# Performance work log

Measured on AMD Instinct MI355X. Metric: run time of the kernel, lower is better.

## Reference

```python
import jax, jax.numpy as jnp
import numpy as np

B, S, C, V, D, H, F, L, SEL = 16, 512, 16, 20000, 512, 8, 2048, 2, 64


def _pos_table(d, max_len):
    # sinusoidal table with a zero row prepended (index 0 = padding)
    pos = np.arange(max_len)[:, None].astype(np.float64)
    j = np.arange(d)[None, :]
    ang = pos / np.power(10000.0, 2 * (j // 2) / d)
    pe = np.zeros((max_len, d))
    pe[:, 0::2] = np.sin(ang[:, 0::2])
    pe[:, 1::2] = np.cos(ang[:, 1::2])
    return jnp.asarray(np.concatenate([np.zeros((1, d)), pe], axis=0), dtype=jnp.float32)


def _ln(x, g, b, eps):
    mu = jnp.mean(x, -1, keepdims=True)
    var = jnp.mean(jnp.square(x - mu), -1, keepdims=True)
    return (x - mu) * jax.lax.rsqrt(var + eps) * g + b


def _forward(event_code, input_len, mask, mask_code, seq_time_step, event_failure_sys, event_failure_user,
             emb, bias_emb, sel_W, sel_b, time_W, time_b,
             Wq, bq, Wk, bk, Wv, bv, Wo, bo, ln1_g, ln1_b, W1, b1, W2, b2, ln2_g, ln2_b):
    Bb, Ss, Cc = event_code.shape
    Dd = emb.shape[1]
    # time feature: 1 - tanh((Dense64(t/7200))^2) -> Dense(D)
    t = seq_time_step[..., None] / 7200.0
    time_feature = (1.0 - jnp.tanh(jnp.square(t @ sel_W + sel_b))) @ time_W + time_b  # [B,S,D]
    # masked sum of per-code embeddings (public-dataset path: failure bits unused)
    act_emb = emb[event_code]                                   # [B,S,C,D]
    out = jnp.sum(act_emb * mask_code, axis=2) + bias_emb       # [B,S,D]
    out = out + time_feature
    # positional encoding gated by real lengths
    pe = _pos_table(Dd, Ss)
    pos = jnp.arange(1, Ss + 1)
    ind_pos = jnp.where(pos[None, :] <= input_len[:, None], pos[None, :], 0)  # [B,S]
    out = out + pe[ind_pos]
    dh = Dd // H
    scale = dh ** -0.5
    for l in range(Wq.shape[0]):
        residual = out
        # NOTE: original uses a raw reshape [B,S,H*dh] -> [B*H,-1,dh]; reproduced exactly.
        q = (out @ Wq[l] + bq[l]).reshape(Bb * H, -1, dh)
        k = (out @ Wk[l] + bk[l]).reshape(Bb * H, -1, dh)
        v = (out @ Wv[l] + bv[l]).reshape(Bb * H, -1, dh)
        # NOTE: original computes tf.where(attn_mask,-inf,attn) but discards the result,
        # so no padding mask is actually applied; reproduced faithfully.
        attn = jax.nn.softmax(jnp.einsum('bqd,bkd->bqk', q, k) * scale, axis=2)
        ctx = jnp.matmul(attn, v).reshape(Bb, -1, H * dh)
        out = _ln(residual + ctx @ Wo[l] + bo[l], ln1_g[l], ln1_b[l], 1e-3)
        ffn = jax.nn.relu(out @ W1[l] + b1[l]) @ W2[l] + b2[l]
        out = _ln(out + ffn, ln2_g[l], ln2_b[l], 1e-6)
    return out


def setup_inputs():
    ks = jax.random.split(jax.random.key(0), 40)
    g = lambda i, shp: jax.random.normal(ks[i], shp, dtype=jnp.float32) * 0.02
    return {
        "event_code": jax.random.randint(ks[0], (B, S, C), 0, V),
        "mask": jnp.ones((B, S), jnp.float32),
        "mask_code": jnp.ones((B, S, C, 1), jnp.float32),
        "seq_time_step": jax.random.uniform(ks[1], (B, S), dtype=jnp.float32) * 7200.0,
        "event_failure_sys": jax.random.uniform(ks[2], (B, S), dtype=jnp.float32),
        "event_failure_user": jax.random.uniform(ks[3], (B, S), dtype=jnp.float32),
        "input_len": jax.random.randint(ks[4], (B,), 1, S + 1),
        "emb": g(5, (V, D)),
        "bias_emb": g(6, (D,)),
        "sel_W": g(7, (1, SEL)), "sel_b": jnp.zeros((SEL,), jnp.float32),
        "time_W": g(8, (SEL, D)), "time_b": jnp.zeros((D,), jnp.float32),
        "Wq": g(9, (L, D, D)), "bq": jnp.zeros((L, D), jnp.float32),
        "Wk": g(10, (L, D, D)), "bk": jnp.zeros((L, D), jnp.float32),
        "Wv": g(11, (L, D, D)), "bv": jnp.zeros((L, D), jnp.float32),
        "Wo": g(12, (L, D, D)), "bo": jnp.zeros((L, D), jnp.float32),
        "ln1_g": jnp.ones((L, D), jnp.float32), "ln1_b": jnp.zeros((L, D), jnp.float32),
        "W1": g(13, (L, D, F)), "b1": jnp.zeros((L, F), jnp.float32),
        "W2": g(14, (L, F, D)), "b2": jnp.zeros((L, D), jnp.float32),
        "ln2_g": jnp.ones((L, D), jnp.float32), "ln2_b": jnp.zeros((L, D), jnp.float32),
    }


def reference(event_code, mask, mask_code, seq_time_step, event_failure_sys, event_failure_user, input_len,
              emb, bias_emb, sel_W, sel_b, time_W, time_b,
              Wq, bq, Wk, bk, Wv, bv, Wo, bo, ln1_g, ln1_b, W1, b1, W2, b2, ln2_g, ln2_b):
    return _forward(event_code, input_len, mask, mask_code, seq_time_step, event_failure_sys, event_failure_user,
                    emb, bias_emb, sel_W, sel_b, time_W, time_b,
                    Wq, bq, Wk, bk, Wv, bv, Wo, bo, ln1_g, ln1_b, W1, b1, W2, b2, ln2_g, ln2_b)
```

## Files before the change

### kernel.cpp

```cpp
#include <hip/hip_runtime.h>
#include <math.h>

#define BB   16
#define SS   512
#define CC   16
#define DD   512
#define DH   64
#define FF   2048
#define LL   2
#define NTOK (BB*SS)
#define NG   (BB*8)
#define GRP  (SS*DH)
#define ST   72

typedef unsigned short u16;
typedef __attribute__((ext_vector_type(8))) short bf16x8;
typedef __attribute__((ext_vector_type(4))) float f32x4;

__device__ __forceinline__ u16 f2bf(float x) {
    unsigned u = __float_as_uint(x);
    u = (u + 0x7fffu + ((u >> 16) & 1u)) >> 16;
    return (u16)u;
}
__device__ __forceinline__ float bf2f(u16 h) {
    return __uint_as_float(((unsigned)h) << 16);
}
__device__ __forceinline__ void gload16(const void* g, void* l) {
    __builtin_amdgcn_global_load_lds((const __attribute__((address_space(1))) void*)g,
                                     (__attribute__((address_space(3))) void*)l, 16, 0, 0);
}

__global__ __launch_bounds__(256) void cvt_weight(
    const float* __restrict__ W, u16* __restrict__ Th, u16* __restrict__ Tl,
    int K, int N)
{
    const long moff = (long)blockIdx.z * K * N;
    W  += moff; Th += moff; Tl += moff;
    const int n0 = blockIdx.x * 32, k0 = blockIdx.y * 32;
    __shared__ float T[32][33];
    const int t = threadIdx.x;

    {
        const int lk = t >> 3, ln4 = (t & 7) * 4;
        float4 w4 = *(const float4*)&W[(long)(k0 + lk) * N + n0 + ln4];
        T[ln4 + 0][lk] = w4.x; T[ln4 + 1][lk] = w4.y;
        T[ln4 + 2][lk] = w4.z; T[ln4 + 3][lk] = w4.w;
    }
    __syncthreads();
    {
        const int nn = t >> 3, kq = (t & 7) * 4;
        float v0 = T[nn][kq + 0], v1 = T[nn][kq + 1];
        float v2 = T[nn][kq + 2], v3 = T[nn][kq + 3];
        ushort4 hh, ll;
        hh.x = f2bf(v0); ll.x = f2bf(v0 - bf2f(hh.x));
        hh.y = f2bf(v1); ll.y = f2bf(v1 - bf2f(hh.y));
        hh.z = f2bf(v2); ll.z = f2bf(v2 - bf2f(hh.z));
        hh.w = f2bf(v3); ll.w = f2bf(v3 - bf2f(hh.w));
        long o = (long)(n0 + nn) * K + k0 + kq;
        *(ushort4*)&Th[o] = hh;
        *(ushort4*)&Tl[o] = ll;
    }
}

__global__ __launch_bounds__(512) void embed_kernel(
    const int*   __restrict__ event_code,
    const float* __restrict__ mask_code,
    const float* __restrict__ seq_time,
    const int*   __restrict__ input_len,
    const float* __restrict__ emb,
    const float* __restrict__ bias_emb,
    const float* __restrict__ sel_W,
    const float* __restrict__ sel_b,
    const float* __restrict__ time_W,
    const float* __restrict__ time_b,
    float* __restrict__ out, u16* __restrict__ oh)
{
    const int tok = blockIdx.x;
    const int b   = tok >> 9;
    const int s   = tok & 511;
    const int d   = threadIdx.x;

    __shared__ float f[64];
    __shared__ int   codes[16];
    __shared__ float mcode[16];

    if (d < 64) {
        float t = seq_time[tok] * (1.0f / 7200.0f);
        float h = t * sel_W[d] + sel_b[d];
        f[d] = 1.0f - tanhf(h * h);
    }
    if (d >= 64 && d < 80) {
        int c = d - 64;
        codes[c] = event_code[tok * CC + c];
        mcode[c] = mask_code[tok * CC + c];
    }
    __syncthreads();

    float acc = bias_emb[d] + time_b[d];
    #pragma unroll
    for (int c = 0; c < CC; ++c)
        acc += emb[(long)codes[c] * DD + d] * mcode[c];
    #pragma unroll 8
    for (int j = 0; j < 64; ++j)
        acc += f[j] * time_W[j * DD + d];

    int pos = s + 1;
    if (pos <= input_len[b]) {
        int p = pos - 1;
        float e    = (float)(d & ~1) * (1.0f / 512.0f);
        float invf = exp2f(-13.287712379549449f * e);
        float ang  = (float)p * invf;
        acc += (d & 1) ? cosf(ang) : sinf(ang);
    }
    long o = (long)tok * DD + d;
    out[o] = acc;
    oh[o] = f2bf(acc);
}

template<int BN, bool RELU, bool RES, int EMIT>
__global__ __launch_bounds__(256) void mgemm(
    const u16* __restrict__ A,
    const u16* __restrict__ Bh, const u16* __restrict__ Bl,
    const float* __restrict__ bias, const float* __restrict__ res,
    float* __restrict__ C, u16* __restrict__ Cb,
    int N, int K)
{
    constexpr int WN = BN / 2;
    constexpr int NI = WN / 16;
    __shared__ __align__(16) u16 A_s[128 * 32];
    __shared__ __align__(16) u16 Bh_s[BN * 32];
    __shared__ __align__(16) u16 Bl_s[BN * 32];

    const int tid  = threadIdx.x;
    const int wid  = tid >> 6, lane = tid & 63;
    const int wr   = wid >> 1, wc = wid & 1;
    const int l4   = lane >> 4, l15 = lane & 15;

    const int bid  = blockIdx.x + gridDim.x * blockIdx.y;
    const int xcd  = bid & 7;
    const int slot = bid >> 3;
    const int ppx  = gridDim.y >> 3;
    const int by   = xcd * ppx + slot / gridDim.x;
    const int bx   = slot % gridDim.x;
    const int m0   = by * 128, n0 = bx * BN;
    const int sr   = lane >> 2, sc = lane & 3;

    f32x4 acc[4][NI];
    #pragma unroll
    for (int mi = 0; mi < 4; ++mi)
        #pragma unroll
        for (int ni = 0; ni < NI; ++ni)
            acc[mi][ni] = (f32x4){0.f, 0.f, 0.f, 0.f};

    for (int k0 = 0; k0 < K; k0 += 32) {
        #pragma unroll
        for (int i = 0; i < 2; ++i) {
            int rr = wid * 32 + i * 16;
            long go = (long)(m0 + rr + sr) * K + k0 + sc * 8;
            gload16(A + go, &A_s[rr * 32]);
        }
        #pragma unroll
        for (int i = 0; i < BN / 64; ++i) {
            int rr = wid * (BN / 4) + i * 16;
            long go = (long)(n0 + rr + sr) * K + k0 + sc * 8;
            gload16(Bh + go, &Bh_s[rr * 32]);
            gload16(Bl + go, &Bl_s[rr * 32]);
        }
        __syncthreads();

        bf16x8 af[4], bh[NI], bl[NI];
        #pragma unroll
        for (int mi = 0; mi < 4; ++mi) {
            int row = wr * 64 + mi * 16 + l15;
            af[mi] = *(const bf16x8*)&A_s[row * 32 + l4 * 8];
        }
        #pragma unroll
        for (int ni = 0; ni < NI; ++ni) {
            int row = wc * WN + ni * 16 + l15;
            bh[ni] = *(const bf16x8*)&Bh_s[row * 32 + l4 * 8];
            bl[ni] = *(const bf16x8*)&Bl_s[row * 32 + l4 * 8];
        }
        #pragma unroll
        for (int mi = 0; mi < 4; ++mi)
            #pragma unroll
            for (int ni = 0; ni < NI; ++ni) {
                acc[mi][ni] = __builtin_amdgcn_mfma_f32_16x16x32_bf16(af[mi], bh[ni], acc[mi][ni], 0, 0, 0);
                acc[mi][ni] = __builtin_amdgcn_mfma_f32_16x16x32_bf16(af[mi], bl[ni], acc[mi][ni], 0, 0, 0);
            }
        __syncthreads();
    }

    #pragma unroll
    for (int mi = 0; mi < 4; ++mi)
        #pragma unroll
        for (int ni = 0; ni < NI; ++ni) {
            int col = n0 + wc * WN + ni * 16 + l15;
            float bv = bias[col];
            #pragma unroll
            for (int r = 0; r < 4; ++r) {
                int row = m0 + wr * 64 + mi * 16 + l4 * 4 + r;
                long off = (long)row * N + col;
                float v = acc[mi][ni][r] + bv;
                if (RES) v += res[off];
                if (RELU) v = fmaxf(v, 0.f);
                if (EMIT == 2) Cb[off] = f2bf(v);
                else           C[off]  = v;
            }
        }
}

__global__ __launch_bounds__(256) void attn_kernel(
    const u16* __restrict__ Qg, const u16* __restrict__ Kg, const u16* __restrict__ Vg,
    u16* __restrict__ Oh)
{
    const int bid = blockIdx.x;
    const int xcd = bid & 7, slot = bid >> 3;
    const int g   = xcd * 16 + (slot >> 3);
    const int qt  = slot & 7;
    const int tid = threadIdx.x;
    const int w   = tid >> 6;
    const int lane = tid & 63;
    const int l4  = lane >> 4, l15 = lane & 15;

    __shared__ __align__(16) u16 Qs[64 * ST];
    __shared__ __align__(16) u16 Ks[64 * ST];
    __shared__ __align__(16) u16 Vt[64 * ST];
    __shared__ __align__(16) u16 Ps[64 * ST];

    const long gbase = (long)g * GRP;

    {
        const u16* src = Qg + gbase + (long)qt * 64 * 64;
        #pragma unroll
        for (int i = 0; i < 2; ++i) {
            int slot2 = tid + i * 256;
            int row = slot2 >> 3, c8 = slot2 & 7;
            *(int4*)&Qs[row * ST + c8 * 8] = *(const int4*)&src[row * 64 + c8 * 8];
        }
    }
    __syncthreads();

    const bf16x8 qf0 = *(const bf16x8*)&Qs[(w * 16 + l15) * ST + l4 * 8];
    const bf16x8 qf1 = *(const bf16x8*)&Qs[(w * 16 + l15) * ST + 32 + l4 * 8];

    f32x4 oacc[4];
    #pragma unroll
    for (int db = 0; db < 4; ++db) oacc[db] = (f32x4){0.f, 0.f, 0.f, 0.f};
    float mrun = -3e38f, lrun = 0.f;

    const int k0t = (tid >> 4) * 4;
    const int d0t = (tid & 15) * 4;

    for (int kt = 0; kt < 8; ++kt) {
        const u16* ksrc = Kg + gbase + (long)kt * 4096;
        const u16* vsrc = Vg + gbase + (long)kt * 4096;
        #pragma unroll
        for (int i = 0; i < 2; ++i) {
            int slot2 = tid + i * 256;
            int row = slot2 >> 3, c8 = slot2 & 7;
            *(int4*)&Ks[row * ST + c8 * 8] = *(const int4*)&ksrc[row * 64 + c8 * 8];
        }
        {
            ushort4 r0 = *(const ushort4*)&vsrc[(k0t + 0) * 64 + d0t];
            ushort4 r1 = *(const ushort4*)&vsrc[(k0t + 1) * 64 + d0t];
            ushort4 r2 = *(const ushort4*)&vsrc[(k0t + 2) * 64 + d0t];
            ushort4 r3 = *(const ushort4*)&vsrc[(k0t + 3) * 64 + d0t];
            ushort4 t0, t1, t2, t3;
            t0.x = r0.x; t0.y = r1.x; t0.z = r2.x; t0.w = r3.x;
            t1.x = r0.y; t1.y = r1.y; t1.z = r2.y; t1.w = r3.y;
            t2.x = r0.z; t2.y = r1.z; t2.z = r2.z; t2.w = r3.z;
            t3.x = r0.w; t3.y = r1.w; t3.z = r2.w; t3.w = r3.w;
            *(ushort4*)&Vt[(d0t + 0) * ST + k0t] = t0;
            *(ushort4*)&Vt[(d0t + 1) * ST + k0t] = t1;
            *(ushort4*)&Vt[(d0t + 2) * ST + k0t] = t2;
            *(ushort4*)&Vt[(d0t + 3) * ST + k0t] = t3;
        }
        __syncthreads();

        f32x4 sacc[4];
        #pragma unroll
        for (int kb = 0; kb < 4; ++kb) {
            bf16x8 a0 = *(const bf16x8*)&Ks[(kb * 16 + l15) * ST + l4 * 8];
            bf16x8 a1 = *(const bf16x8*)&Ks[(kb * 16 + l15) * ST + 32 + l4 * 8];
            f32x4 z = (f32x4){0.f, 0.f, 0.f, 0.f};
            z = __builtin_amdgcn_mfma_f32_16x16x32_bf16(a0, qf0, z, 0, 0, 0);
            z = __builtin_amdgcn_mfma_f32_16x16x32_bf16(a1, qf1, z, 0, 0, 0);
            sacc[kb] = z;
        }

        float pm = -3e38f;
        #pragma unroll
        for (int kb = 0; kb < 4; ++kb)
            #pragma unroll
            for (int r = 0; r < 4; ++r)
                pm = fmaxf(pm, sacc[kb][r]);
        pm *= 0.125f;
        pm = fmaxf(pm, __shfl_xor(pm, 16));
        pm = fmaxf(pm, __shfl_xor(pm, 32));
        float mn   = fmaxf(mrun, pm);
        float corr = __expf(mrun - mn);
        float psum = 0.f;
        u16 pb[16];
        #pragma unroll
        for (int kb = 0; kb < 4; ++kb)
            #pragma unroll
            for (int r = 0; r < 4; ++r) {
                float p = __expf(sacc[kb][r] * 0.125f - mn);
                u16 b = f2bf(p);
                pb[kb * 4 + r] = b;
                psum += bf2f(b);
            }
        psum += __shfl_xor(psum, 16);
        psum += __shfl_xor(psum, 32);
        lrun = lrun * corr + psum;
        mrun = mn;

        #pragma unroll
        for (int kb = 0; kb < 4; ++kb)
            #pragma unroll
            for (int r = 0; r < 4; ++r)
                Ps[(w * 16 + l15) * ST + kb * 16 + l4 * 4 + r] = pb[kb * 4 + r];

        float cr[4];
        #pragma unroll
        for (int r = 0; r < 4; ++r) cr[r] = __shfl(corr, l4 * 4 + r);
        #pragma unroll
        for (int db = 0; db < 4; ++db)
            #pragma unroll
            for (int r = 0; r < 4; ++r)
                oacc[db][r] *= cr[r];

        asm volatile("s_waitcnt lgkmcnt(0)" ::: "memory");
        __builtin_amdgcn_sched_barrier(0);
        bf16x8 pa0 = *(const bf16x8*)&Ps[(w * 16 + l15) * ST + l4 * 8];
        bf16x8 pa1 = *(const bf16x8*)&Ps[(w * 16 + l15) * ST + 32 + l4 * 8];
        #pragma unroll
        for (int db = 0; db < 4; ++db) {
            bf16x8 v0 = *(const bf16x8*)&Vt[(db * 16 + l15) * ST + l4 * 8];
            bf16x8 v1 = *(const bf16x8*)&Vt[(db * 16 + l15) * ST + 32 + l4 * 8];
            oacc[db] = __builtin_amdgcn_mfma_f32_16x16x32_bf16(pa0, v0, oacc[db], 0, 0, 0);
            oacc[db] = __builtin_amdgcn_mfma_f32_16x16x32_bf16(pa1, v1, oacc[db], 0, 0, 0);
        }
        __syncthreads();
    }

    float li[4];
    #pragma unroll
    for (int r = 0; r < 4; ++r) li[r] = 1.0f / __shfl(lrun, l4 * 4 + r);
    #pragma unroll
    for (int db = 0; db < 4; ++db)
        #pragma unroll
        for (int r = 0; r < 4; ++r) {
            float val = oacc[db][r] * li[r];
            long addr = gbase + (long)(qt * 64 + w * 16 + l4 * 4 + r) * 64 + db * 16 + l15;
            Oh[addr] = f2bf(val);
        }
}

__global__ __launch_bounds__(256) void ln_kernel(
    const float* __restrict__ X,
    const float* __restrict__ gam,
    const float* __restrict__ bet,
    float* __restrict__ Y, u16* __restrict__ Yh,
    float eps)
{
    const int row = blockIdx.x;
    const int tid = threadIdx.x;
    const float* x = X + (long)row * DD;

    float x0 = x[tid], x1 = x[tid + 256];
    __shared__ float ws4[4];
    const int wid = tid >> 6, lane = tid & 63;

    float sum = x0 + x1;
    #pragma unroll
    for (int off = 32; off > 0; off >>= 1) sum += __shfl_down(sum, off, 64);
    if (lane == 0) ws4[wid] = sum;
    __syncthreads();
    float mean = (ws4[0] + ws4[1] + ws4[2] + ws4[3]) * (1.0f / 512.0f);
    __syncthreads();

    float d0 = x0 - mean, d1 = x1 - mean;
    float s2 = d0 * d0 + d1 * d1;
    #pragma unroll
    for (int off = 32; off > 0; off >>= 1) s2 += __shfl_down(s2, off, 64);
    if (lane == 0) ws4[wid] = s2;
    __syncthreads();
    float var = (ws4[0] + ws4[1] + ws4[2] + ws4[3]) * (1.0f / 512.0f);
    float inv = rsqrtf(var + eps);

    float o0 = d0 * inv * gam[tid]       + bet[tid];
    float o1 = d1 * inv * gam[tid + 256] + bet[tid + 256];
    long b0 = (long)row * DD + tid;
    Y[b0] = o0;  Y[b0 + 256] = o1;
    Yh[b0] = f2bf(o0);
    Yh[b0 + 256] = f2bf(o1);
}

extern "C" void kernel_launch(void* const* d_in, const int* in_sizes, int n_in,
                              void* d_out, int out_size, void* d_ws, size_t ws_size,
                              hipStream_t stream)
{
    const int*   event_code = (const int*)  d_in[0];
    const float* mask_code  = (const float*)d_in[2];
    const float* seq_time   = (const float*)d_in[3];
    const int*   input_len  = (const int*)  d_in[6];
    const float* emb        = (const float*)d_in[7];
    const float* bias_emb   = (const float*)d_in[8];
    const float* sel_W      = (const float*)d_in[9];
    const float* sel_b      = (const float*)d_in[10];
    const float* time_W     = (const float*)d_in[11];
    const float* time_b     = (const float*)d_in[12];
    const float* Wq  = (const float*)d_in[13];
    const float* bq  = (const float*)d_in[14];
    const float* Wk  = (const float*)d_in[15];
    const float* bk  = (const float*)d_in[16];
    const float* Wv  = (const float*)d_in[17];
    const float* bv  = (const float*)d_in[18];
    const float* Wo  = (const float*)d_in[19];
    const float* bo  = (const float*)d_in[20];
    const float* ln1g = (const float*)d_in[21];
    const float* ln1b = (const float*)d_in[22];
    const float* W1  = (const float*)d_in[23];
    const float* b1  = (const float*)d_in[24];
    const float* W2  = (const float*)d_in[25];
    const float* b2  = (const float*)d_in[26];
    const float* ln2g = (const float*)d_in[27];
    const float* ln2b = (const float*)d_in[28];

    float* ws = (float*)d_ws;
    const long ND = (long)NTOK * DD;
    const long NF = (long)NTOK * FF;
    float* x = ws;
    float* y = ws + ND;
    u16* q16 = (u16*)(ws + 2 * ND);
    u16* k16 = q16 + ND;
    u16* v16 = k16 + ND;
    u16* a16 = v16 + ND;
    u16* h16 = a16 + ND;
    u16* wq_h = h16 + NF;
    const long SZQ = (long)LL * DD * DD, SZF = (long)LL * DD * FF;
    u16* wq_l = wq_h + SZQ;
    u16* wk_h = wq_l + SZQ;  u16* wk_l = wk_h + SZQ;
    u16* wv_h = wk_l + SZQ;  u16* wv_l = wv_h + SZQ;
    u16* wo_h = wv_l + SZQ;  u16* wo_l = wo_h + SZQ;
    u16* w1_h = wo_l + SZQ;  u16* w1_l = w1_h + SZF;
    u16* w2_h = w1_l + SZF;  u16* w2_l = w2_h + SZF;

    cvt_weight<<<dim3(DD/32, DD/32, LL), 256, 0, stream>>>(Wq, wq_h, wq_l, DD, DD);
    cvt_weight<<<dim3(DD/32, DD/32, LL), 256, 0, stream>>>(Wk, wk_h, wk_l, DD, DD);
    cvt_weight<<<dim3(DD/32, DD/32, LL), 256, 0, stream>>>(Wv, wv_h, wv_l, DD, DD);
    cvt_weight<<<dim3(DD/32, DD/32, LL), 256, 0, stream>>>(Wo, wo_h, wo_l, DD, DD);
    cvt_weight<<<dim3(FF/32, DD/32, LL), 256, 0, stream>>>(W1, w1_h, w1_l, DD, FF);
    cvt_weight<<<dim3(DD/32, FF/32, LL), 256, 0, stream>>>(W2, w2_h, w2_l, FF, DD);

    embed_kernel<<<NTOK, 512, 0, stream>>>(event_code, mask_code, seq_time, input_len,
                                           emb, bias_emb, sel_W, sel_b, time_W, time_b,
                                           x, a16);

    const dim3 gN512(DD / 64, NTOK / 128);
    const dim3 gN2048(FF / 128, NTOK / 128);

    for (int l = 0; l < LL; ++l) {
        const u16* qh = wq_h + (long)l * DD * DD;  const u16* ql = wq_l + (long)l * DD * DD;
        const u16* kh = wk_h + (long)l * DD * DD;  const u16* kl = wk_l + (long)l * DD * DD;
        const u16* vh = wv_h + (long)l * DD * DD;  const u16* vl = wv_l + (long)l * DD * DD;
        const u16* oh = wo_h + (long)l * DD * DD;  const u16* ol = wo_l + (long)l * DD * DD;
        const u16* f1h = w1_h + (long)l * DD * FF; const u16* f1l = w1_l + (long)l * DD * FF;
        const u16* f2h = w2_h + (long)l * FF * DD; const u16* f2l = w2_l + (long)l * FF * DD;

        mgemm<64,false,false,2><<<gN512, 256, 0, stream>>>(a16, qh, ql, bq + l*DD, nullptr, nullptr, q16, DD, DD);
        mgemm<64,false,false,2><<<gN512, 256, 0, stream>>>(a16, kh, kl, bk + l*DD, nullptr, nullptr, k16, DD, DD);
        mgemm<64,false,false,2><<<gN512, 256, 0, stream>>>(a16, vh, vl, bv + l*DD, nullptr, nullptr, v16, DD, DD);

        attn_kernel<<<NG * 8, 256, 0, stream>>>(q16, k16, v16, a16);

        mgemm<64,false,true,0><<<gN512, 256, 0, stream>>>(a16, oh, ol, bo + l*DD, x, y, nullptr, DD, DD);
        ln_kernel<<<NTOK, 256, 0, stream>>>(y, ln1g + l*DD, ln1b + l*DD, y, a16, 1e-3f);

        mgemm<128,true,false,2><<<gN2048, 256, 0, stream>>>(a16, f1h, f1l, b1 + l*FF, nullptr, nullptr, h16, FF, DD);
        mgemm<64,false,true,0><<<gN512, 256, 0, stream>>>(h16, f2h, f2l, b2 + l*DD, y, x, nullptr, DD, FF);

        float* lnout = (l == LL - 1) ? (float*)d_out : x;
        ln_kernel<<<NTOK, 256, 0, stream>>>(x, ln2g + l*DD, ln2b + l*DD, lnout, a16, 1e-6f);
    }
}
```

Measured before the change: 617.0 us.

## Fuse QKV GEMMs, double-buffer GEMM LDS loads, use bf16 embedding table

The separate Q, K and V projection GEMMs become one N=1536 GEMM over a packed weight, with a segmented epilogue that routes columns to the three outputs. The GEMM main loop gains double-buffered LDS staging with explicit vmcnt waits, so the next tile's global loads overlap the MFMA work. The Q/K/V/O weight conversions merge into one launch. The embedding table is converted to bf16 and the embed kernel processes two features per thread with vector loads. Converting the 20000x512 table every call adds a full pass over it, and bf16 embeddings lose precision compared with the fp32 gather.

```diff
diff --git a/kernel.cpp b/kernel.cpp
--- a/kernel.cpp
+++ b/kernel.cpp
@@ -8,6 +8,7 @@
 #define DH   64
 #define FF   2048
 #define LL   2
+#define VV   20000
 #define NTOK (BB*SS)
 #define NG   (BB*8)
 #define GRP  (SS*DH)
@@ -30,16 +31,58 @@
                                      (__attribute__((address_space(3))) void*)l, 16, 0, 0);
 }
 
+__global__ __launch_bounds__(256) void cvt_qkvo(
+    const float* __restrict__ Wq, const float* __restrict__ Wk,
+    const float* __restrict__ Wv, const float* __restrict__ Wo,
+    u16* __restrict__ qkv_h, u16* __restrict__ qkv_l,
+    u16* __restrict__ o_h,   u16* __restrict__ o_l)
+{
+    const int z = blockIdx.z;
+    const int which = z >> 1, l = z & 1;
+    const float* W = (which == 0) ? Wq : (which == 1) ? Wk : (which == 2) ? Wv : Wo;
+    W += (long)l * DD * DD;
+    u16 *Th, *Tl;
+    if (which < 3) {
+        long off = (long)l * 1536 * DD + (long)which * DD * DD;
+        Th = qkv_h + off; Tl = qkv_l + off;
+    } else {
+        long off = (long)l * DD * DD;
+        Th = o_h + off;   Tl = o_l + off;
+    }
+    const int n0 = blockIdx.x * 32, k0 = blockIdx.y * 32;
+    __shared__ float T[32][33];
+    const int t = threadIdx.x;
+    {
+        const int lk = t >> 3, ln4 = (t & 7) * 4;
+        float4 w4 = *(const float4*)&W[(long)(k0 + lk) * DD + n0 + ln4];
+        T[ln4 + 0][lk] = w4.x; T[ln4 + 1][lk] = w4.y;
+        T[ln4 + 2][lk] = w4.z; T[ln4 + 3][lk] = w4.w;
+    }
+    __syncthreads();
+    {
+        const int nn = t >> 3, kq = (t & 7) * 4;
+        float v0 = T[nn][kq + 0], v1 = T[nn][kq + 1];
+        float v2 = T[nn][kq + 2], v3 = T[nn][kq + 3];
+        ushort4 hh, ll;
+        hh.x = f2bf(v0); ll.x = f2bf(v0 - bf2f(hh.x));
+        hh.y = f2bf(v1); ll.y = f2bf(v1 - bf2f(hh.y));
+        hh.z = f2bf(v2); ll.z = f2bf(v2 - bf2f(hh.z));
+        hh.w = f2bf(v3); ll.w = f2bf(v3 - bf2f(hh.w));
+        long o = (long)(n0 + nn) * DD + k0 + kq;
+        *(ushort4*)&Th[o] = hh;
+        *(ushort4*)&Tl[o] = ll;
+    }
+}
+
 __global__ __launch_bounds__(256) void cvt_weight(
     const float* __restrict__ W, u16* __restrict__ Th, u16* __restrict__ Tl,
     int K, int N)
 {
     const long moff = (long)blockIdx.z * K * N;
-    W  += moff; Th += moff; Tl += moff;
+    W += moff; Th += moff; Tl += moff;
     const int n0 = blockIdx.x * 32, k0 = blockIdx.y * 32;
     __shared__ float T[32][33];
     const int t = threadIdx.x;
-
     {
         const int lk = t >> 3, ln4 = (t & 7) * 4;
         float4 w4 = *(const float4*)&W[(long)(k0 + lk) * N + n0 + ln4];
@@ -62,12 +105,22 @@
     }
 }
 
-__global__ __launch_bounds__(512) void embed_kernel(
+__global__ __launch_bounds__(256) void cvt_emb(const float* __restrict__ E,
+                                               u16* __restrict__ E16)
+{
+    long i = ((long)blockIdx.x * 256 + threadIdx.x) * 4;
+    float4 v = *(const float4*)&E[i];
+    ushort4 o;
+    o.x = f2bf(v.x); o.y = f2bf(v.y); o.z = f2bf(v.z); o.w = f2bf(v.w);
+    *(ushort4*)&E16[i] = o;
+}
+
+__global__ __launch_bounds__(256) void embed_kernel(
     const int*   __restrict__ event_code,
     const float* __restrict__ mask_code,
     const float* __restrict__ seq_time,
     const int*   __restrict__ input_len,
-    const float* __restrict__ emb,
+    const u16*   __restrict__ emb16,
     const float* __restrict__ bias_emb,
     const float* __restrict__ sel_W,
     const float* __restrict__ sel_b,
@@ -78,58 +131,73 @@
     const int tok = blockIdx.x;
     const int b   = tok >> 9;
     const int s   = tok & 511;
-    const int d   = threadIdx.x;
+    const int t2  = threadIdx.x;
+    const int d   = t2 * 2;
 
     __shared__ float f[64];
     __shared__ int   codes[16];
     __shared__ float mcode[16];
 
-    if (d < 64) {
+    if (t2 < 64) {
         float t = seq_time[tok] * (1.0f / 7200.0f);
-        float h = t * sel_W[d] + sel_b[d];
-        f[d] = 1.0f - tanhf(h * h);
-    }
-    if (d >= 64 && d < 80) {
-        int c = d - 64;
+        float h = t * sel_W[t2] + sel_b[t2];
+        f[t2] = 1.0f - tanhf(h * h);
+    }
+    if (t2 >= 64 && t2 < 80) {
+        int c = t2 - 64;
         codes[c] = event_code[tok * CC + c];
         mcode[c] = mask_code[tok * CC + c];
     }
     __syncthreads();
 
-    float acc = bias_emb[d] + time_b[d];
-    #pragma unroll
-    for (int c = 0; c < CC; ++c)
-        acc += emb[(long)codes[c] * DD + d] * mcode[c];
+    float acc0 = bias_emb[d]     + time_b[d];
+    float acc1 = bias_emb[d + 1] + time_b[d + 1];
+    #pragma unroll
+    for (int c = 0; c < CC; ++c) {
+        unsigned pk = *(const unsigned*)&emb16[(long)codes[c] * DD + d];
+        acc0 += bf2f((u16)(pk & 0xffffu)) * mcode[c];
+        acc1 += bf2f((u16)(pk >> 16))     * mcode[c];
+    }
     #pragma unroll 8
-    for (int j = 0; j < 64; ++j)
-        acc += f[j] * time_W[j * DD + d];
+    for (int j = 0; j < 64; ++j) {
+        float2 tw = *(const float2*)&time_W[j * DD + d];
+        acc0 += f[j] * tw.x;
+        acc1 += f[j] * tw.y;
+    }
 
     int pos = s + 1;
     if (pos <= input_len[b]) {
         int p = pos - 1;
-        float e    = (float)(d & ~1) * (1.0f / 512.0f);
+        float e    = (float)d * (1.0f / 512.0f);
         float invf = exp2f(-13.287712379549449f * e);
         float ang  = (float)p * invf;
-        acc += (d & 1) ? cosf(ang) : sinf(ang);
+        acc0 += sinf(ang);
+        acc1 += cosf(ang);
     }
     long o = (long)tok * DD + d;
-    out[o] = acc;
-    oh[o] = f2bf(acc);
-}
-
-template<int BN, bool RELU, bool RES, int EMIT>
+    float2 o2; o2.x = acc0; o2.y = acc1;
+    *(float2*)&out[o] = o2;
+    unsigned pk = (unsigned)f2bf(acc0) | ((unsigned)f2bf(acc1) << 16);
+    *(unsigned*)&oh[o] = pk;
+}
+
+template<int BN, bool RELU, bool RES, int EMIT, bool SEG3>
 __global__ __launch_bounds__(256) void mgemm(
     const u16* __restrict__ A,
     const u16* __restrict__ Bh, const u16* __restrict__ Bl,
-    const float* __restrict__ bias, const float* __restrict__ res,
-    float* __restrict__ C, u16* __restrict__ Cb,
+    const float* __restrict__ bias0, const float* __restrict__ bias1,
+    const float* __restrict__ bias2,
+    const float* __restrict__ res,
+    float* __restrict__ C,
+    u16* __restrict__ O0, u16* __restrict__ O1, u16* __restrict__ O2,
     int N, int K)
 {
-    constexpr int WN = BN / 2;
-    constexpr int NI = WN / 16;
-    __shared__ __align__(16) u16 A_s[128 * 32];
-    __shared__ __align__(16) u16 Bh_s[BN * 32];
-    __shared__ __align__(16) u16 Bl_s[BN * 32];
+    constexpr int WN  = BN / 2;
+    constexpr int NI  = WN / 16;
+    constexpr int LPW = 2 + 2 * (BN / 64);
+    __shared__ __align__(16) u16 A_s[2][128 * 32];
+    __shared__ __align__(16) u16 Bh_s[2][BN * 32];
+    __shared__ __align__(16) u16 Bl_s[2][BN * 32];
 
     const int tid  = threadIdx.x;
     const int wid  = tid >> 6, lane = tid & 63;
@@ -145,41 +213,57 @@
     const int m0   = by * 128, n0 = bx * BN;
     const int sr   = lane >> 2, sc = lane & 3;
 
-    f32x4 acc[4][NI];
-    #pragma unroll
-    for (int mi = 0; mi < 4; ++mi)
-        #pragma unroll
-        for (int ni = 0; ni < NI; ++ni)
-            acc[mi][ni] = (f32x4){0.f, 0.f, 0.f, 0.f};
-
-    for (int k0 = 0; k0 < K; k0 += 32) {
+    auto STAGE = [&](int bufi, int k0) {
         #pragma unroll
         for (int i = 0; i < 2; ++i) {
             int rr = wid * 32 + i * 16;
             long go = (long)(m0 + rr + sr) * K + k0 + sc * 8;
-            gload16(A + go, &A_s[rr * 32]);
+            gload16(A + go, &A_s[bufi][rr * 32]);
         }
         #pragma unroll
         for (int i = 0; i < BN / 64; ++i) {
             int rr = wid * (BN / 4) + i * 16;
             long go = (long)(n0 + rr + sr) * K + k0 + sc * 8;
-            gload16(Bh + go, &Bh_s[rr * 32]);
-            gload16(Bl + go, &Bl_s[rr * 32]);
-        }
-        __syncthreads();
+            gload16(Bh + go, &Bh_s[bufi][rr * 32]);
+            gload16(Bl + go, &Bl_s[bufi][rr * 32]);
+        }
+    };
+
+    f32x4 acc[4][NI];
+    #pragma unroll
+    for (int mi = 0; mi < 4; ++mi)
+        #pragma unroll
+        for (int ni = 0; ni < NI; ++ni)
+            acc[mi][ni] = (f32x4){0.f, 0.f, 0.f, 0.f};
+
+    STAGE(0, 0);
+    const int nt = K / 32;
+    for (int t = 0; t < nt; ++t) {
+        const int cur = t & 1;
+        if (t + 1 < nt) {
+            STAGE(cur ^ 1, (t + 1) * 32);
+            asm volatile("s_waitcnt vmcnt(%0)" :: "i"(LPW) : "memory");
+        } else {
+            asm volatile("s_waitcnt vmcnt(0)" ::: "memory");
+        }
+        __builtin_amdgcn_s_barrier();
 
         bf16x8 af[4], bh[NI], bl[NI];
         #pragma unroll
         for (int mi = 0; mi < 4; ++mi) {
             int row = wr * 64 + mi * 16 + l15;
-            af[mi] = *(const bf16x8*)&A_s[row * 32 + l4 * 8];
+            af[mi] = *(const bf16x8*)&A_s[cur][row * 32 + l4 * 8];
         }
         #pragma unroll
         for (int ni = 0; ni < NI; ++ni) {
             int row = wc * WN + ni * 16 + l15;
-            bh[ni] = *(const bf16x8*)&Bh_s[row * 32 + l4 * 8];
-            bl[ni] = *(const bf16x8*)&Bl_s[row * 32 + l4 * 8];
-        }
+            bh[ni] = *(const bf16x8*)&Bh_s[cur][row * 32 + l4 * 8];
+            bl[ni] = *(const bf16x8*)&Bl_s[cur][row * 32 + l4 * 8];
+        }
+        asm volatile("s_waitcnt lgkmcnt(0)" ::: "memory");
+        __builtin_amdgcn_sched_barrier(0);
+        __builtin_amdgcn_s_barrier();
+
         #pragma unroll
         for (int mi = 0; mi < 4; ++mi)
             #pragma unroll
@@ -187,23 +271,27 @@
                 acc[mi][ni] = __builtin_amdgcn_mfma_f32_16x16x32_bf16(af[mi], bh[ni], acc[mi][ni], 0, 0, 0);
                 acc[mi][ni] = __builtin_amdgcn_mfma_f32_16x16x32_bf16(af[mi], bl[ni], acc[mi][ni], 0, 0, 0);
             }
-        __syncthreads();
     }
 
     #pragma unroll
     for (int mi = 0; mi < 4; ++mi)
         #pragma unroll
         for (int ni = 0; ni < NI; ++ni) {
-            int col = n0 + wc * WN + ni * 16 + l15;
-            float bv = bias[col];
+            int colg = n0 + wc * WN + ni * 16 + l15;
+            int seg  = SEG3 ? (colg >> 9) : 0;
+            int coll = SEG3 ? (colg & 511) : colg;
+            const float* bp = SEG3 ? (seg == 0 ? bias0 : seg == 1 ? bias1 : bias2) : bias0;
+            u16* op = SEG3 ? (seg == 0 ? O0 : seg == 1 ? O1 : O2) : O0;
+            const int ost = SEG3 ? 512 : N;
+            float bv = bp[coll];
             #pragma unroll
             for (int r = 0; r < 4; ++r) {
                 int row = m0 + wr * 64 + mi * 16 + l4 * 4 + r;
-                long off = (long)row * N + col;
+                long off = (long)row * ost + coll;
                 float v = acc[mi][ni][r] + bv;
                 if (RES) v += res[off];
                 if (RELU) v = fmaxf(v, 0.f);
-                if (EMIT == 2) Cb[off] = f2bf(v);
+                if (EMIT == 2) op[off] = f2bf(v);
                 else           C[off]  = v;
             }
         }
@@ -438,48 +526,52 @@
     u16* v16 = k16 + ND;
     u16* a16 = v16 + ND;
     u16* h16 = a16 + ND;
-    u16* wq_h = h16 + NF;
+    u16* e16 = h16 + NF;
+    u16* wqkv_h = e16 + (long)VV * DD;
+    const long SZ3 = (long)LL * 1536 * DD;
     const long SZQ = (long)LL * DD * DD, SZF = (long)LL * DD * FF;
-    u16* wq_l = wq_h + SZQ;
-    u16* wk_h = wq_l + SZQ;  u16* wk_l = wk_h + SZQ;
-    u16* wv_h = wk_l + SZQ;  u16* wv_l = wv_h + SZQ;
-    u16* wo_h = wv_l + SZQ;  u16* wo_l = wo_h + SZQ;
-    u16* w1_h = wo_l + SZQ;  u16* w1_l = w1_h + SZF;
-    u16* w2_h = w1_l + SZF;  u16* w2_l = w2_h + SZF;
-
-    cvt_weight<<<dim3(DD/32, DD/32, LL), 256, 0, stream>>>(Wq, wq_h, wq_l, DD, DD);
-    cvt_weight<<<dim3(DD/32, DD/32, LL), 256, 0, stream>>>(Wk, wk_h, wk_l, DD, DD);
-    cvt_weight<<<dim3(DD/32, DD/32, LL), 256, 0, stream>>>(Wv, wv_h, wv_l, DD, DD);
-    cvt_weight<<<dim3(DD/32, DD/32, LL), 256, 0, stream>>>(Wo, wo_h, wo_l, DD, DD);
+    u16* wqkv_l = wqkv_h + SZ3;
+    u16* wo_h = wqkv_l + SZ3;  u16* wo_l = wo_h + SZQ;
+    u16* w1_h = wo_l + SZQ;    u16* w1_l = w1_h + SZF;
+    u16* w2_h = w1_l + SZF;    u16* w2_l = w2_h + SZF;
+
+    cvt_qkvo<<<dim3(16, 16, 8), 256, 0, stream>>>(Wq, Wk, Wv, Wo, wqkv_h, wqkv_l, wo_h, wo_l);
     cvt_weight<<<dim3(FF/32, DD/32, LL), 256, 0, stream>>>(W1, w1_h, w1_l, DD, FF);
     cvt_weight<<<dim3(DD/32, FF/32, LL), 256, 0, stream>>>(W2, w2_h, w2_l, FF, DD);
-
-    embed_kernel<<<NTOK, 512, 0, stream>>>(event_code, mask_code, seq_time, input_len,
-                                           emb, bias_emb, sel_W, sel_b, time_W, time_b,
+    cvt_emb<<<(VV * DD) / 1024, 256, 0, stream>>>(emb, e16);
+
+    embed_kernel<<<NTOK, 256, 0, stream>>>(event_code, mask_code, seq_time, input_len,
+                                           e16, bias_emb, sel_W, sel_b, time_W, time_b,
                                            x, a16);
 
+    const dim3 gQKV(1536 / 64, NTOK / 128);
     const dim3 gN512(DD / 64, NTOK / 128);
     const dim3 gN2048(FF / 128, NTOK / 128);
 
     for (int l = 0; l < LL; ++l) {
-        const u16* qh = wq_h + (long)l * DD * DD;  const u16* ql = wq_l + (long)l * DD * DD;
-        const u16* kh = wk_h + (long)l * DD * DD;  const u16* kl = wk_l + (long)l * DD * DD;
-        const u16* vh = wv_h + (long)l * DD * DD;  const u16* vl = wv_l + (long)l * DD * DD;
+        const u16* qkvh = wqkv_h + (long)l * 1536 * DD;
+        const u16* qkvl = wqkv_l + (long)l * 1536 * DD;
         const u16* oh = wo_h + (long)l * DD * DD;  const u16* ol = wo_l + (long)l * DD * DD;
         const u16* f1h = w1_h + (long)l * DD * FF; const u16* f1l = w1_l + (long)l * DD * FF;
         const u16* f2h = w2_h + (long)l * FF * DD; const u16* f2l = w2_l + (long)l * FF * DD;
 
-        mgemm<64,false,false,2><<<gN512, 256, 0, stream>>>(a16, qh, ql, bq + l*DD, nullptr, nullptr, q16, DD, DD);
-        mgemm<64,false,false,2><<<gN512, 256, 0, stream>>>(a16, kh, kl, bk + l*DD, nullptr, nullptr, k16, DD, DD);
-        mgemm<64,false,false,2><<<gN512, 256, 0, stream>>>(a16, vh, vl, bv + l*DD, nullptr, nullptr, v16, DD, DD);
+        mgemm<64,false,false,2,true><<<gQKV, 256, 0, stream>>>(
+            a16, qkvh, qkvl, bq + l*DD, bk + l*DD, bv + l*DD, nullptr,
+            nullptr, q16, k16, v16, 1536, DD);
 
         attn_kernel<<<NG * 8, 256, 0, stream>>>(q16, k16, v16, a16);
 
-        mgemm<64,false,true,0><<<gN512, 256, 0, stream>>>(a16, oh, ol, bo + l*DD, x, y, nullptr, DD, DD);
+        mgemm<64,false,true,0,false><<<gN512, 256, 0, stream>>>(
+            a16, oh, ol, bo + l*DD, nullptr, nullptr, x,
+            y, nullptr, nullptr, nullptr, DD, DD);
         ln_kernel<<<NTOK, 256, 0, stream>>>(y, ln1g + l*DD, ln1b + l*DD, y, a16, 1e-3f);
 
-        mgemm<128,true,false,2><<<gN2048, 256, 0, stream>>>(a16, f1h, f1l, b1 + l*FF, nullptr, nullptr, h16, FF, DD);
-        mgemm<64,false,true,0><<<gN512, 256, 0, stream>>>(h16, f2h, f2l, b2 + l*DD, y, x, nullptr, DD, FF);
+        mgemm<128,true,false,2,false><<<gN2048, 256, 0, stream>>>(
+            a16, f1h, f1l, b1 + l*FF, nullptr, nullptr, nullptr,
+            nullptr, h16, nullptr, nullptr, FF, DD);
+        mgemm<64,false,true,0,false><<<gN512, 256, 0, stream>>>(
+            h16, f2h, f2l, b2 + l*DD, nullptr, nullptr, y,
+            x, nullptr, nullptr, nullptr, DD, FF);
 
         float* lnout = (l == LL - 1) ? (float*)d_out : x;
         ln_kernel<<<NTOK, 256, 0, stream>>>(x, ln2g + l*DD, ln2b + l*DD, lnout, a16, 1e-6f);
```

Result: faster. 596.2 us (-3.4%).
